# Performance work log

Hardware: AMD Instinct MI355X
Metric: run time of the kernel (lower is better)

## Reference

```python
import jax, jax.numpy as jnp
import numpy as np

B, N_O, N_Q = 2, 512, 512
POS_DIM, LATENT, HEADS, HEAD_DIM, OUT_DIM = 3, 256, 8, 32, 128
HD = HEADS * HEAD_DIM  # == LATENT here


def _lin(key, fan_in, fan_out):
    return jax.random.normal(key, (fan_in, fan_out), jnp.float32) / np.sqrt(fan_in)


def setup_inputs() -> dict:
    key = jax.random.key(0)
    ks = jax.random.split(key, 12)
    return {
        'h_obs': jax.random.normal(ks[0], (B, N_O, LATENT), jnp.float32),
        'pos_obs': jax.random.uniform(ks[1], (B, N_O, POS_DIM), jnp.float32),
        'pos_query': jax.random.uniform(ks[2], (B, N_Q, POS_DIM), jnp.float32),
        'fw1': _lin(ks[3], LATENT, LATENT), 'fb1': jnp.zeros((LATENT,), jnp.float32),
        'fw2': _lin(ks[4], LATENT, HD), 'fb2': jnp.zeros((HD,), jnp.float32),
        'log_sigma': jnp.zeros((HEADS,), jnp.float32),
        'kw1': _lin(ks[5], POS_DIM * 3, LATENT), 'kb1': jnp.zeros((LATENT,), jnp.float32),
        'kw2': _lin(ks[6], LATENT, HEADS), 'kb2': jnp.zeros((HEADS,), jnp.float32),
        'ow': _lin(ks[7], HD, OUT_DIM), 'ob': jnp.zeros((OUT_DIM,), jnp.float32),
        'vw': _lin(ks[8], HD, OUT_DIM), 'vb': jnp.zeros((OUT_DIM,), jnp.float32),
    }


def reference(h_obs, pos_obs, pos_query, fw1, fb1, fw2, fb2, log_sigma,
              kw1, kb1, kw2, kb2, ow, ob, vw, vb):
    Bv, No, _ = h_obs.shape
    Nq = pos_query.shape[1]
    # feature net -> values [B, H, N_o, D]
    v = jax.nn.relu(h_obs @ fw1 + fb1) @ fw2 + fb2
    v = v.reshape(Bv, No, HEADS, HEAD_DIM).transpose(0, 2, 1, 3)
    # pairwise relative positions [B, Nq, No, P]
    pos_q = pos_query[:, :, None, :]
    pos_o = pos_obs[:, None, :, :]
    rel = pos_q - pos_o
    dist2 = jnp.sum(rel ** 2, axis=-1)  # [B, Nq, No]
    sigma = jnp.exp(log_sigma)[None, :, None, None]
    rbf = jnp.exp(-dist2[:, None] / (sigma ** 2 + 1e-6))  # [B, H, Nq, No]
    # kernel MLP on concatenated pairwise positions [B, Nq, No, 3P] -> [B, H, Nq, No]
    ki = jnp.concatenate([
        jnp.broadcast_to(pos_q, (Bv, Nq, No, POS_DIM)),
        jnp.broadcast_to(pos_o, (Bv, Nq, No, POS_DIM)),
        rel], axis=-1)
    delta = (jax.nn.relu(ki @ kw1 + kb1) @ kw2 + kb2).transpose(0, 3, 1, 2)
    logits = jnp.log(rbf + 1e-8) + delta
    weights = jax.nn.softmax(logits, axis=-1)  # [B, H, Nq, No]
    # weighted mean over observations
    v_mean = jnp.einsum('bhqo,bhod->bhqd', weights, v)  # [B, H, Nq, D]
    h_query = v_mean.transpose(0, 2, 1, 3).reshape(Bv, Nq, HD)
    # weighted variance: sum_o w * (v_o - v_mean)^2
    residual = v[:, :, None, :, :] - v_mean[:, :, :, None, :]  # [B, H, Nq, No, D]
    var = jnp.sum(weights[..., None] * residual ** 2, axis=3)  # [B, H, Nq, D]
    var = var.transpose(0, 2, 1, 3).reshape(Bv, Nq, HD)
    mean = h_query @ ow + ob
    var_out = jax.nn.softplus(var @ vw + vb)
    return (mean, var_out)
```

## Files before the change

### kernel.cpp

```cpp
#include <hip/hip_runtime.h>
#include <math.h>

#define NB 2
#define NO 512
#define NQ 512
#define OUT_DIM 128
#define LPAD 516

typedef __attribute__((ext_vector_type(8))) _Float16 half8;
typedef __attribute__((ext_vector_type(4))) _Float16 half4;
typedef __attribute__((ext_vector_type(4))) float f32x4;

__device__ __forceinline__ float softplus_f(float x) {
  return x > 0.0f ? x + log1pf(expf(-x)) : log1pf(expf(x));
}
__device__ __forceinline__ int cvt2h(float x, float y) {
  return __builtin_bit_cast(int, __builtin_amdgcn_cvt_pkrtz(x, y));
}

__global__ __launch_bounds__(1024) void prep_kernel(
    const float* __restrict__ h_obs, const float* __restrict__ fw1,
    const float* __restrict__ fb1, const float* __restrict__ fw2,
    const float* __restrict__ fb2, const float* __restrict__ pos_obs,
    const float* __restrict__ kw1,
    _Float16* __restrict__ VT,
    _Float16* __restrict__ VT2,
    _Float16* __restrict__ AO_h)
{
  if (blockIdx.x < 256) {
    __shared__ float s_red[4][4][256];
    __shared__ float s_hid[4][256];
    const int n  = threadIdx.x & 255;
    const int ks = threadIdx.x >> 8;
    const int r0 = blockIdx.x * 4;
    const int k0 = ks * 64;
    float a0 = 0.f, a1 = 0.f, a2 = 0.f, a3 = 0.f;
    #pragma unroll 8
    for (int kk = 0; kk < 64; ++kk) {
      int k = k0 + kk;
      float w = fw1[k * 256 + n];
      a0 = fmaf(h_obs[(r0 + 0) * 256 + k], w, a0);
      a1 = fmaf(h_obs[(r0 + 1) * 256 + k], w, a1);
      a2 = fmaf(h_obs[(r0 + 2) * 256 + k], w, a2);
      a3 = fmaf(h_obs[(r0 + 3) * 256 + k], w, a3);
    }
    s_red[ks][0][n] = a0; s_red[ks][1][n] = a1;
    s_red[ks][2][n] = a2; s_red[ks][3][n] = a3;
    __syncthreads();
    if (ks == 0) {
      float bb = fb1[n];
      #pragma unroll
      for (int r = 0; r < 4; ++r) {
        float v = s_red[0][r][n] + s_red[1][r][n] + s_red[2][r][n] + s_red[3][r][n] + bb;
        s_hid[r][n] = fmaxf(v, 0.f);
      }
    }
    __syncthreads();
    float c0 = 0.f, c1 = 0.f, c2 = 0.f, c3 = 0.f;
    #pragma unroll 8
    for (int kk = 0; kk < 64; ++kk) {
      int k = k0 + kk;
      float w = fw2[k * 256 + n];
      c0 = fmaf(s_hid[0][k], w, c0);
      c1 = fmaf(s_hid[1][k], w, c1);
      c2 = fmaf(s_hid[2][k], w, c2);
      c3 = fmaf(s_hid[3][k], w, c3);
    }
    __syncthreads();
    s_red[ks][0][n] = c0; s_red[ks][1][n] = c1;
    s_red[ks][2][n] = c2; s_red[ks][3][n] = c3;
    __syncthreads();
    if (ks == 0) {
      float bb = fb2[n];
      float vr[4];
      #pragma unroll
      for (int r = 0; r < 4; ++r)
        vr[r] = s_red[0][r][n] + s_red[1][r][n] + s_red[2][r][n] + s_red[3][r][n] + bb;
      const int h  = n >> 5, d = n & 31;
      const int bb_ = r0 >> 9, o0 = r0 & 511;
      half4 pv, pv2;
      #pragma unroll
      for (int r = 0; r < 4; ++r) {
        pv[r]  = (_Float16)vr[r];
        pv2[r] = (_Float16)(vr[r] * vr[r]);
      }
      const size_t idx = ((size_t)((bb_ * 8 + h) * 32 + d)) * 512 + o0;
      *(half4*)(VT  + idx) = pv;
      *(half4*)(VT2 + idx) = pv2;
    }
  } else {
    const int i  = blockIdx.x - 256;
    const int b  = i >> 7;
    const int og = i & 127;
    const int ol = threadIdx.x >> 8;
    const int j  = threadIdx.x & 255;
    const int o  = og * 4 + ol;
    float c0 = kw1[3 * 256 + j] - kw1[6 * 256 + j];
    float c1 = kw1[4 * 256 + j] - kw1[7 * 256 + j];
    float c2 = kw1[5 * 256 + j] - kw1[8 * 256 + j];
    const float* p = pos_obs + ((size_t)(b * NO + o)) * 3;
    AO_h[(size_t)(b * NO + o) * 256 + j] =
        (_Float16)(fmaf(p[0], c0, fmaf(p[1], c1, p[2] * c2)));
  }
}

__global__ __launch_bounds__(512, 4) void attn_fused(
    const _Float16* __restrict__ VT,
    const _Float16* __restrict__ VT2,
    const _Float16* __restrict__ AO_h,
    const float* __restrict__ kw1,
    const float* __restrict__ kb1,
    const float* __restrict__ kw2,
    const float* __restrict__ kb2,
    const float* __restrict__ log_sigma,
    const float* __restrict__ pos_obs,
    const float* __restrict__ pos_query,
    const float* __restrict__ ow, const float* __restrict__ obias,
    const float* __restrict__ vw, const float* __restrict__ vbias,
    float* __restrict__ out)
{
  __shared__ __align__(16) float s_logits[2][8 * LPAD];
  __shared__ half8 s_Bh[512];
  __shared__ __align__(16) float s_pool[2048];

  _Float16* s_aq2 = (_Float16*)s_pool;
  float*    s_hv  = s_pool;
  float*    s_pred = s_pool + 1024;

  const int t   = threadIdx.x;
  const int bq0 = blockIdx.x * 2;
  const int b   = bq0 >> 9;

  float pqx[2], pqy[2], pqz[2];
  #pragma unroll
  for (int q = 0; q < 2; ++q) {
    pqx[q] = pos_query[(bq0 + q) * 3 + 0];
    pqy[q] = pos_query[(bq0 + q) * 3 + 1];
    pqz[q] = pos_query[(bq0 + q) * 3 + 2];
  }
  {
    const int q = t >> 8, j = t & 255;
    float c0 = kw1[0 * 256 + j] + kw1[6 * 256 + j];
    float c1 = kw1[1 * 256 + j] + kw1[7 * 256 + j];
    float c2 = kw1[2 * 256 + j] + kw1[8 * 256 + j];
    s_aq2[q * 256 + j] = (_Float16)
        fmaf(pqx[q], c0, fmaf(pqy[q], c1, fmaf(pqz[q], c2, kb1[j])));
  }
  {
    const int o = t;
    const float* p = pos_obs + (size_t)(b * NO + o) * 3;
    float px = p[0], py = p[1], pz = p[2];
    float d2q[2];
    #pragma unroll
    for (int q = 0; q < 2; ++q) {
      float r0 = pqx[q] - px, r1 = pqy[q] - py, r2 = pqz[q] - pz;
      d2q[q] = r0 * r0 + r1 * r1 + r2 * r2;
    }
    #pragma unroll
    for (int h = 0; h < 8; ++h) {
      float sg  = __expf(log_sigma[h]);
      float inv = 1.0f / (sg * sg + 1e-6f);
      float kbv = kb2[h];
      s_logits[0][h * LPAD + o] = __logf(__expf(-d2q[0] * inv) + 1e-8f) + kbv;
      s_logits[1][h * LPAD + o] = __logf(__expf(-d2q[1] * inv) + 1e-8f) + kbv;
    }
  }
  {
    const int kstep = t >> 6, lane = t & 63;
    const int nh = lane & 15;
    const int kb_ = kstep * 32 + ((lane >> 4) & 3) * 8;
    half8 b8;
    #pragma unroll
    for (int i = 0; i < 8; ++i) {
      float v = (nh < 8) ? kw2[(kb_ + i) * 8 + nh] : 0.f;
      b8[i] = (_Float16)v;
    }
    s_Bh[kstep * 64 + lane] = b8;
  }
  __syncthreads();

  {
    const int wave = t >> 6, lane = t & 63;
    const int quad = lane >> 4, mrow = lane & 15;
    const int tb   = wave * 4;
    f32x4 C[2][4];
    #pragma unroll
    for (int q = 0; q < 2; ++q)
      #pragma unroll
      for (int jt = 0; jt < 4; ++jt) C[q][jt] = (f32x4){0.f, 0.f, 0.f, 0.f};

    const half8 z8 = {0, 0, 0, 0, 0, 0, 0, 0};
    for (int kstep = 0; kstep < 8; ++kstep) {
      const int koff = kstep * 32 + quad * 8;
      half8 aq0 = *(const half8*)(s_aq2 + koff);
      half8 aq1 = *(const half8*)(s_aq2 + 256 + koff);
      half8 bh  = s_Bh[kstep * 64 + lane];
      #pragma unroll
      for (int jt = 0; jt < 4; ++jt) {
        const int o = (tb + jt) * 16 + mrow;
        half8 ao = *(const half8*)(AO_h + ((size_t)(b * NO + o) << 8) + koff);
        half8 a0 = __builtin_elementwise_max(aq0 + ao, z8);
        half8 a1 = __builtin_elementwise_max(aq1 + ao, z8);
        C[0][jt] = __builtin_amdgcn_mfma_f32_16x16x32_f16(a0, bh, C[0][jt], 0, 0, 0);
        C[1][jt] = __builtin_amdgcn_mfma_f32_16x16x32_f16(a1, bh, C[1][jt], 0, 0, 0);
      }
    }
    const int hh = lane & 15;
    if (hh < 8) {
      #pragma unroll
      for (int q = 0; q < 2; ++q)
        #pragma unroll
        for (int jt = 0; jt < 4; ++jt) {
          const int ob2 = (tb + jt) * 16 + quad * 4;
          #pragma unroll
          for (int r = 0; r < 4; ++r)
            s_logits[q][hh * LPAD + ob2 + r] += C[q][jt][r];
        }
    }
  }
  __syncthreads();

  {
    const int h = t >> 6, lane = t & 63;
    float invq[2];
    #pragma unroll
    for (int q = 0; q < 2; ++q) {
      float* pl = &s_logits[q][h * LPAD];
      float l8[8];
      float m = -1e30f;
      #pragma unroll
      for (int k = 0; k < 8; ++k) {
        l8[k] = pl[k * 64 + lane];
        m = fmaxf(m, l8[k]);
      }
      #pragma unroll
      for (int off = 32; off >= 1; off >>= 1) m = fmaxf(m, __shfl_xor(m, off, 64));
      float s = 0.f;
      #pragma unroll
      for (int k = 0; k < 8; ++k) {
        float p = __expf(l8[k] - m);
        pl[k * 64 + lane] = p;
        s += p;
      }
      #pragma unroll
      for (int off = 32; off >= 1; off >>= 1) s += __shfl_xor(s, off, 64);
      invq[q] = 1.0f / s;
    }
    const int nq = lane & 15, kg = lane >> 4, dl = lane & 15;
    const size_t vbase = ((size_t)(b * 8 + h) * 32 + dl) * 512;
    const _Float16* vt1 = VT  + vbase;
    const _Float16* vt2 = VT2 + vbase;
    const float* P = &s_logits[nq & 1][h * LPAD];
    f32x4 Cm0 = {0.f,0.f,0.f,0.f}, Cm1 = Cm0, Cv0 = Cm0, Cv1 = Cm0;
    #pragma unroll 4
    for (int ks = 0; ks < 16; ++ks) {
      const int ob = ks * 32 + kg * 8;
      float4 p0 = *(const float4*)(P + ob);
      float4 p1 = *(const float4*)(P + ob + 4);
      int4 bi;
      bi.x = cvt2h(p0.x, p0.y); bi.y = cvt2h(p0.z, p0.w);
      bi.z = cvt2h(p1.x, p1.y); bi.w = cvt2h(p1.z, p1.w);
      half8 bh = __builtin_bit_cast(half8, bi);
      half8 am0 = *(const half8*)(vt1 + ob);
      half8 am1 = *(const half8*)(vt1 + 8192 + ob);
      half8 av0 = *(const half8*)(vt2 + ob);
      half8 av1 = *(const half8*)(vt2 + 8192 + ob);
      Cm0 = __builtin_amdgcn_mfma_f32_16x16x32_f16(am0, bh, Cm0, 0, 0, 0);
      Cm1 = __builtin_amdgcn_mfma_f32_16x16x32_f16(am1, bh, Cm1, 0, 0, 0);
      Cv0 = __builtin_amdgcn_mfma_f32_16x16x32_f16(av0, bh, Cv0, 0, 0, 0);
      Cv1 = __builtin_amdgcn_mfma_f32_16x16x32_f16(av1, bh, Cv1, 0, 0, 0);
    }
    if (nq < 2) {
      const float iv = nq ? invq[1] : invq[0];
      const int dbase = h * 32 + kg * 4;
      f32x4 m0, v0, m1, v1;
      #pragma unroll
      for (int r = 0; r < 4; ++r) {
        float a = Cm0[r] * iv;
        m0[r] = a; v0[r] = fmaxf(Cv0[r] * iv - a * a, 0.f);
        float c = Cm1[r] * iv;
        m1[r] = c; v1[r] = fmaxf(Cv1[r] * iv - c * c, 0.f);
      }
      *(f32x4*)(s_hv + (nq * 2 + 0) * 256 + dbase)      = m0;
      *(f32x4*)(s_hv + (nq * 2 + 1) * 256 + dbase)      = v0;
      *(f32x4*)(s_hv + (nq * 2 + 0) * 256 + dbase + 16) = m1;
      *(f32x4*)(s_hv + (nq * 2 + 1) * 256 + dbase + 16) = v1;
    }
  }
  __syncthreads();

  {
    const int ks = t >> 8, mode = (t >> 7) & 1, n = t & 127;
    const float* W  = mode ? vw : ow;
    const float* X0 = s_hv + mode * 256;
    const float* X1 = s_hv + (2 + mode) * 256;
    float a0 = 0.f, a1 = 0.f;
    const int k0 = ks * 128;
    #pragma unroll 4
    for (int k = k0; k < k0 + 128; k += 4) {
      float4 x0 = *(const float4*)&X0[k];
      float4 x1 = *(const float4*)&X1[k];
      float w0 = W[(k + 0) * 128 + n];
      float w1 = W[(k + 1) * 128 + n];
      float w2 = W[(k + 2) * 128 + n];
      float w3 = W[(k + 3) * 128 + n];
      a0 = fmaf(x0.x, w0, a0); a1 = fmaf(x1.x, w0, a1);
      a0 = fmaf(x0.y, w1, a0); a1 = fmaf(x1.y, w1, a1);
      a0 = fmaf(x0.z, w2, a0); a1 = fmaf(x1.z, w2, a1);
      a0 = fmaf(x0.w, w3, a0); a1 = fmaf(x1.w, w3, a1);
    }
    s_pred[((ks * 2 + mode) * 2 + 0) * 128 + n] = a0;
    s_pred[((ks * 2 + mode) * 2 + 1) * 128 + n] = a1;
  }
  __syncthreads();
  {
    const int q = t >> 8, mode = (t >> 7) & 1, n = t & 127;
    float v = s_pred[((0 * 2 + mode) * 2 + q) * 128 + n]
            + s_pred[((1 * 2 + mode) * 2 + q) * 128 + n]
            + (mode ? vbias[n] : obias[n]);
    if (mode) v = softplus_f(v);
    out[(size_t)mode * (NB * NQ * OUT_DIM) + (size_t)(bq0 + q) * OUT_DIM + n] = v;
  }
}

extern "C" void kernel_launch(void* const* d_in, const int* in_sizes, int n_in,
                              void* d_out, int out_size, void* d_ws, size_t ws_size,
                              hipStream_t stream)
{
  const float* h_obs     = (const float*)d_in[0];
  const float* pos_obs   = (const float*)d_in[1];
  const float* pos_query = (const float*)d_in[2];
  const float* fw1       = (const float*)d_in[3];
  const float* fb1       = (const float*)d_in[4];
  const float* fw2       = (const float*)d_in[5];
  const float* fb2       = (const float*)d_in[6];
  const float* log_sigma = (const float*)d_in[7];
  const float* kw1       = (const float*)d_in[8];
  const float* kb1       = (const float*)d_in[9];
  const float* kw2       = (const float*)d_in[10];
  const float* kb2       = (const float*)d_in[11];
  const float* ow        = (const float*)d_in[12];
  const float* ob        = (const float*)d_in[13];
  const float* vw        = (const float*)d_in[14];
  const float* vb        = (const float*)d_in[15];

  float* out = (float*)d_out;
  _Float16* ws = (_Float16*)d_ws;

  _Float16* AO_h = ws;
  _Float16* VT   = ws + 262144;
  _Float16* VT2  = ws + 524288;

  prep_kernel<<<512, 1024, 0, stream>>>(h_obs, fw1, fb1, fw2, fb2,
                                        pos_obs, kw1, VT, VT2, AO_h);
  attn_fused<<<NB * NQ / 2, 512, 0, stream>>>(VT, VT2, AO_h, kw1, kb1, kw2, kb2,
                                              log_sigma, pos_obs, pos_query,
                                              ow, ob, vw, vb, out);
}
```

Measured before the change: 155.2 us.

## Recompute obs kernel features and V^2 on the fly, stage V via async LDS loads

Drops the precomputed AO_h and VT2 workspace buffers. The per-observation kernel-MLP term is now rebuilt in registers from pos_obs and coefficients held in shared memory, and V squared is computed in registers from V. Probabilities are stored once as fp16 in shared memory, and V tiles are streamed with global_load_lds into a ring of buffers paced by explicit vmcnt waits. This cuts global traffic and the prep kernel's work, but adds half-precision ALU work, an extra barrier, and fragile manual wait counts.

```diff
diff --git a/kernel.cpp b/kernel.cpp
--- a/kernel.cpp
+++ b/kernel.cpp
@@ -14,100 +14,85 @@
 __device__ __forceinline__ float softplus_f(float x) {
   return x > 0.0f ? x + log1pf(expf(-x)) : log1pf(expf(x));
 }
-__device__ __forceinline__ int cvt2h(float x, float y) {
-  return __builtin_bit_cast(int, __builtin_amdgcn_cvt_pkrtz(x, y));
+__device__ __forceinline__ half8 splat8(_Float16 v) {
+  return (half8){v, v, v, v, v, v, v, v};
+}
+__device__ __forceinline__ half8 fma8(half8 a, half8 b, half8 c) {
+  return __builtin_elementwise_fma(a, b, c);
+}
+__device__ __forceinline__ half8 max8(half8 a, half8 b) {
+  return __builtin_elementwise_max(a, b);
+}
+__device__ __forceinline__ void gll16(const void* g, void* l) {
+  __builtin_amdgcn_global_load_lds(
+      (const __attribute__((address_space(1))) unsigned int*)g,
+      (__attribute__((address_space(3))) unsigned int*)l, 16, 0, 0);
 }
 
 __global__ __launch_bounds__(1024) void prep_kernel(
     const float* __restrict__ h_obs, const float* __restrict__ fw1,
     const float* __restrict__ fb1, const float* __restrict__ fw2,
-    const float* __restrict__ fb2, const float* __restrict__ pos_obs,
-    const float* __restrict__ kw1,
-    _Float16* __restrict__ VT,
-    _Float16* __restrict__ VT2,
-    _Float16* __restrict__ AO_h)
+    const float* __restrict__ fb2, _Float16* __restrict__ VT)
 {
-  if (blockIdx.x < 256) {
-    __shared__ float s_red[4][4][256];
-    __shared__ float s_hid[4][256];
-    const int n  = threadIdx.x & 255;
-    const int ks = threadIdx.x >> 8;
-    const int r0 = blockIdx.x * 4;
-    const int k0 = ks * 64;
-    float a0 = 0.f, a1 = 0.f, a2 = 0.f, a3 = 0.f;
-    #pragma unroll 8
-    for (int kk = 0; kk < 64; ++kk) {
-      int k = k0 + kk;
-      float w = fw1[k * 256 + n];
-      a0 = fmaf(h_obs[(r0 + 0) * 256 + k], w, a0);
-      a1 = fmaf(h_obs[(r0 + 1) * 256 + k], w, a1);
-      a2 = fmaf(h_obs[(r0 + 2) * 256 + k], w, a2);
-      a3 = fmaf(h_obs[(r0 + 3) * 256 + k], w, a3);
-    }
-    s_red[ks][0][n] = a0; s_red[ks][1][n] = a1;
-    s_red[ks][2][n] = a2; s_red[ks][3][n] = a3;
-    __syncthreads();
-    if (ks == 0) {
-      float bb = fb1[n];
-      #pragma unroll
-      for (int r = 0; r < 4; ++r) {
-        float v = s_red[0][r][n] + s_red[1][r][n] + s_red[2][r][n] + s_red[3][r][n] + bb;
-        s_hid[r][n] = fmaxf(v, 0.f);
-      }
-    }
-    __syncthreads();
-    float c0 = 0.f, c1 = 0.f, c2 = 0.f, c3 = 0.f;
-    #pragma unroll 8
-    for (int kk = 0; kk < 64; ++kk) {
-      int k = k0 + kk;
-      float w = fw2[k * 256 + n];
-      c0 = fmaf(s_hid[0][k], w, c0);
-      c1 = fmaf(s_hid[1][k], w, c1);
-      c2 = fmaf(s_hid[2][k], w, c2);
-      c3 = fmaf(s_hid[3][k], w, c3);
-    }
-    __syncthreads();
-    s_red[ks][0][n] = c0; s_red[ks][1][n] = c1;
-    s_red[ks][2][n] = c2; s_red[ks][3][n] = c3;
-    __syncthreads();
-    if (ks == 0) {
-      float bb = fb2[n];
-      float vr[4];
-      #pragma unroll
-      for (int r = 0; r < 4; ++r)
-        vr[r] = s_red[0][r][n] + s_red[1][r][n] + s_red[2][r][n] + s_red[3][r][n] + bb;
-      const int h  = n >> 5, d = n & 31;
-      const int bb_ = r0 >> 9, o0 = r0 & 511;
-      half4 pv, pv2;
-      #pragma unroll
-      for (int r = 0; r < 4; ++r) {
-        pv[r]  = (_Float16)vr[r];
-        pv2[r] = (_Float16)(vr[r] * vr[r]);
-      }
-      const size_t idx = ((size_t)((bb_ * 8 + h) * 32 + d)) * 512 + o0;
-      *(half4*)(VT  + idx) = pv;
-      *(half4*)(VT2 + idx) = pv2;
-    }
-  } else {
-    const int i  = blockIdx.x - 256;
-    const int b  = i >> 7;
-    const int og = i & 127;
-    const int ol = threadIdx.x >> 8;
-    const int j  = threadIdx.x & 255;
-    const int o  = og * 4 + ol;
-    float c0 = kw1[3 * 256 + j] - kw1[6 * 256 + j];
-    float c1 = kw1[4 * 256 + j] - kw1[7 * 256 + j];
-    float c2 = kw1[5 * 256 + j] - kw1[8 * 256 + j];
-    const float* p = pos_obs + ((size_t)(b * NO + o)) * 3;
-    AO_h[(size_t)(b * NO + o) * 256 + j] =
-        (_Float16)(fmaf(p[0], c0, fmaf(p[1], c1, p[2] * c2)));
+  __shared__ float s_red[4][4][256];
+  __shared__ float s_hid[4][256];
+  const int n  = threadIdx.x & 255;
+  const int ks = threadIdx.x >> 8;
+  const int r0 = blockIdx.x * 4;
+  const int k0 = ks * 64;
+  float a0 = 0.f, a1 = 0.f, a2 = 0.f, a3 = 0.f;
+  #pragma unroll 8
+  for (int kk = 0; kk < 64; ++kk) {
+    int k = k0 + kk;
+    float w = fw1[k * 256 + n];
+    a0 = fmaf(h_obs[(r0 + 0) * 256 + k], w, a0);
+    a1 = fmaf(h_obs[(r0 + 1) * 256 + k], w, a1);
+    a2 = fmaf(h_obs[(r0 + 2) * 256 + k], w, a2);
+    a3 = fmaf(h_obs[(r0 + 3) * 256 + k], w, a3);
+  }
+  s_red[ks][0][n] = a0; s_red[ks][1][n] = a1;
+  s_red[ks][2][n] = a2; s_red[ks][3][n] = a3;
+  __syncthreads();
+  if (ks == 0) {
+    float bb = fb1[n];
+    #pragma unroll
+    for (int r = 0; r < 4; ++r) {
+      float v = s_red[0][r][n] + s_red[1][r][n] + s_red[2][r][n] + s_red[3][r][n] + bb;
+      s_hid[r][n] = fmaxf(v, 0.f);
+    }
+  }
+  __syncthreads();
+  float c0 = 0.f, c1 = 0.f, c2 = 0.f, c3 = 0.f;
+  #pragma unroll 8
+  for (int kk = 0; kk < 64; ++kk) {
+    int k = k0 + kk;
+    float w = fw2[k * 256 + n];
+    c0 = fmaf(s_hid[0][k], w, c0);
+    c1 = fmaf(s_hid[1][k], w, c1);
+    c2 = fmaf(s_hid[2][k], w, c2);
+    c3 = fmaf(s_hid[3][k], w, c3);
+  }
+  __syncthreads();
+  s_red[ks][0][n] = c0; s_red[ks][1][n] = c1;
+  s_red[ks][2][n] = c2; s_red[ks][3][n] = c3;
+  __syncthreads();
+  if (ks == 0) {
+    float bb = fb2[n];
+    float vr[4];
+    #pragma unroll
+    for (int r = 0; r < 4; ++r)
+      vr[r] = s_red[0][r][n] + s_red[1][r][n] + s_red[2][r][n] + s_red[3][r][n] + bb;
+    const int h  = n >> 5, d = n & 31;
+    const int bb_ = r0 >> 9, o0 = r0 & 511;
+    half4 pv;
+    #pragma unroll
+    for (int r = 0; r < 4; ++r) pv[r] = (_Float16)vr[r];
+    *(half4*)(VT + ((size_t)((bb_ * 8 + h) * 32 + d)) * 512 + o0) = pv;
   }
 }
 
 __global__ __launch_bounds__(512, 4) void attn_fused(
     const _Float16* __restrict__ VT,
-    const _Float16* __restrict__ VT2,
-    const _Float16* __restrict__ AO_h,
     const float* __restrict__ kw1,
     const float* __restrict__ kb1,
     const float* __restrict__ kw2,
@@ -120,11 +105,14 @@
     float* __restrict__ out)
 {
   __shared__ __align__(16) float s_logits[2][8 * LPAD];
+  __shared__ __align__(16) _Float16 s_P16[2][8][520];
   __shared__ half8 s_Bh[512];
   __shared__ __align__(16) float s_pool[2048];
+  __shared__ __align__(16) float s_po[3][516];
+  __shared__ __align__(16) _Float16 s_co[3][264];
 
   _Float16* s_aq2 = (_Float16*)s_pool;
-  float*    s_hv  = s_pool;
+  float*    s_hv   = s_pool;
   float*    s_pred = s_pool + 1024;
 
   const int t   = threadIdx.x;
@@ -146,10 +134,17 @@
     s_aq2[q * 256 + j] = (_Float16)
         fmaf(pqx[q], c0, fmaf(pqy[q], c1, fmaf(pqz[q], c2, kb1[j])));
   }
+  if (t < 256) {
+    const int j = t;
+    s_co[0][j] = (_Float16)(kw1[3 * 256 + j] - kw1[6 * 256 + j]);
+    s_co[1][j] = (_Float16)(kw1[4 * 256 + j] - kw1[7 * 256 + j]);
+    s_co[2][j] = (_Float16)(kw1[5 * 256 + j] - kw1[8 * 256 + j]);
+  }
   {
     const int o = t;
     const float* p = pos_obs + (size_t)(b * NO + o) * 3;
     float px = p[0], py = p[1], pz = p[2];
+    s_po[0][o] = px; s_po[1][o] = py; s_po[2][o] = pz;
     float d2q[2];
     #pragma unroll
     for (int q = 0; q < 2; ++q) {
@@ -183,6 +178,14 @@
     const int wave = t >> 6, lane = t & 63;
     const int quad = lane >> 4, mrow = lane & 15;
     const int tb   = wave * 4;
+    _Float16 pxh[4], pyh[4], pzh[4];
+    #pragma unroll
+    for (int jt = 0; jt < 4; ++jt) {
+      const int o = (tb + jt) * 16 + mrow;
+      pxh[jt] = (_Float16)s_po[0][o];
+      pyh[jt] = (_Float16)s_po[1][o];
+      pzh[jt] = (_Float16)s_po[2][o];
+    }
     f32x4 C[2][4];
     #pragma unroll
     for (int q = 0; q < 2; ++q)
@@ -190,17 +193,21 @@
       for (int jt = 0; jt < 4; ++jt) C[q][jt] = (f32x4){0.f, 0.f, 0.f, 0.f};
 
     const half8 z8 = {0, 0, 0, 0, 0, 0, 0, 0};
+    #pragma unroll
     for (int kstep = 0; kstep < 8; ++kstep) {
       const int koff = kstep * 32 + quad * 8;
+      half8 c0 = *(const half8*)&s_co[0][koff];
+      half8 c1 = *(const half8*)&s_co[1][koff];
+      half8 c2 = *(const half8*)&s_co[2][koff];
       half8 aq0 = *(const half8*)(s_aq2 + koff);
       half8 aq1 = *(const half8*)(s_aq2 + 256 + koff);
       half8 bh  = s_Bh[kstep * 64 + lane];
       #pragma unroll
       for (int jt = 0; jt < 4; ++jt) {
-        const int o = (tb + jt) * 16 + mrow;
-        half8 ao = *(const half8*)(AO_h + ((size_t)(b * NO + o) << 8) + koff);
-        half8 a0 = __builtin_elementwise_max(aq0 + ao, z8);
-        half8 a1 = __builtin_elementwise_max(aq1 + ao, z8);
+        half8 ao = fma8(splat8(pxh[jt]), c0,
+                   fma8(splat8(pyh[jt]), c1, splat8(pzh[jt]) * c2));
+        half8 a0 = max8(aq0 + ao, z8);
+        half8 a1 = max8(aq1 + ao, z8);
         C[0][jt] = __builtin_amdgcn_mfma_f32_16x16x32_f16(a0, bh, C[0][jt], 0, 0, 0);
         C[1][jt] = __builtin_amdgcn_mfma_f32_16x16x32_f16(a1, bh, C[1][jt], 0, 0, 0);
       }
@@ -239,39 +246,48 @@
       #pragma unroll
       for (int k = 0; k < 8; ++k) {
         float p = __expf(l8[k] - m);
-        pl[k * 64 + lane] = p;
         s += p;
+        s_P16[q][h][k * 64 + lane] = (_Float16)p;
       }
       #pragma unroll
       for (int off = 32; off >= 1; off >>= 1) s += __shfl_xor(s, off, 64);
       invq[q] = 1.0f / s;
     }
-    const int nq = lane & 15, kg = lane >> 4, dl = lane & 15;
-    const size_t vbase = ((size_t)(b * 8 + h) * 32 + dl) * 512;
-    const _Float16* vt1 = VT  + vbase;
-    const _Float16* vt2 = VT2 + vbase;
-    const float* P = &s_logits[nq & 1][h * LPAD];
-    f32x4 Cm0 = {0.f,0.f,0.f,0.f}, Cm1 = Cm0, Cv0 = Cm0, Cv1 = Cm0;
-    #pragma unroll 4
+    __syncthreads();
+
+    const int kg = lane >> 4, dl = lane & 15;
+    char* stg = (char*)s_logits + h * 4096;
+    const _Float16* vt = VT + ((size_t)(b * 8 + h) << 14);
+    const _Float16* vsrc = vt + (lane >> 1) * 512 + (lane & 1) * 8;
+    #define STAGE(j) gll16(vsrc + (j) * 16, stg + ((j) & 3) * 1024)
+    STAGE(0); STAGE(1); STAGE(2); STAGE(3);
+
+    const _Float16* pB = &s_P16[lane & 1][h][0];
+    f32x4 Cm0 = {0.f, 0.f, 0.f, 0.f}, Cm1 = Cm0, Cv0 = Cm0, Cv1 = Cm0;
+    #pragma unroll
     for (int ks = 0; ks < 16; ++ks) {
-      const int ob = ks * 32 + kg * 8;
-      float4 p0 = *(const float4*)(P + ob);
-      float4 p1 = *(const float4*)(P + ob + 4);
-      int4 bi;
-      bi.x = cvt2h(p0.x, p0.y); bi.y = cvt2h(p0.z, p0.w);
-      bi.z = cvt2h(p1.x, p1.y); bi.w = cvt2h(p1.z, p1.w);
-      half8 bh = __builtin_bit_cast(half8, bi);
-      half8 am0 = *(const half8*)(vt1 + ob);
-      half8 am1 = *(const half8*)(vt1 + 8192 + ob);
-      half8 av0 = *(const half8*)(vt2 + ob);
-      half8 av1 = *(const half8*)(vt2 + 8192 + ob);
-      Cm0 = __builtin_amdgcn_mfma_f32_16x16x32_f16(am0, bh, Cm0, 0, 0, 0);
-      Cm1 = __builtin_amdgcn_mfma_f32_16x16x32_f16(am1, bh, Cm1, 0, 0, 0);
-      Cv0 = __builtin_amdgcn_mfma_f32_16x16x32_f16(av0, bh, Cv0, 0, 0, 0);
-      Cv1 = __builtin_amdgcn_mfma_f32_16x16x32_f16(av1, bh, Cv1, 0, 0, 0);
-    }
+      if (ks < 15) asm volatile("s_waitcnt vmcnt(2)" ::: "memory");
+      else         asm volatile("s_waitcnt vmcnt(0)" ::: "memory");
+      const char* bufc = stg + ((2 * ks + (kg >> 1)) & 3) * 1024
+                       + dl * 32 + (kg & 1) * 16;
+      half8 am0 = *(const half8*)(bufc);
+      half8 am1 = *(const half8*)(bufc + 512);
+      half8 pb  = *(const half8*)(pB + ks * 32 + kg * 8);
+      half8 av0 = am0 * am0;
+      half8 av1 = am1 * am1;
+      Cm0 = __builtin_amdgcn_mfma_f32_16x16x32_f16(am0, pb, Cm0, 0, 0, 0);
+      Cm1 = __builtin_amdgcn_mfma_f32_16x16x32_f16(am1, pb, Cm1, 0, 0, 0);
+      Cv0 = __builtin_amdgcn_mfma_f32_16x16x32_f16(av0, pb, Cv0, 0, 0, 0);
+      Cv1 = __builtin_amdgcn_mfma_f32_16x16x32_f16(av1, pb, Cv1, 0, 0, 0);
+      if (ks < 14) {
+        asm volatile("s_waitcnt lgkmcnt(0)" ::: "memory");
+        STAGE(2 * ks + 4); STAGE(2 * ks + 5);
+      }
+    }
+    #undef STAGE
+    const int nq = lane & 15;
     if (nq < 2) {
-      const float iv = nq ? invq[1] : invq[0];
+      const float iv = invq[nq];
       const int dbase = h * 32 + kg * 4;
       f32x4 m0, v0, m1, v1;
       #pragma unroll
@@ -345,15 +361,10 @@
   const float* vb        = (const float*)d_in[15];
 
   float* out = (float*)d_out;
-  _Float16* ws = (_Float16*)d_ws;
-
-  _Float16* AO_h = ws;
-  _Float16* VT   = ws + 262144;
-  _Float16* VT2  = ws + 524288;
-
-  prep_kernel<<<512, 1024, 0, stream>>>(h_obs, fw1, fb1, fw2, fb2,
-                                        pos_obs, kw1, VT, VT2, AO_h);
-  attn_fused<<<NB * NQ / 2, 512, 0, stream>>>(VT, VT2, AO_h, kw1, kb1, kw2, kb2,
+  _Float16* VT = (_Float16*)d_ws;
+
+  prep_kernel<<<256, 1024, 0, stream>>>(h_obs, fw1, fb1, fw2, fb2, VT);
+  attn_fused<<<NB * NQ / 2, 512, 0, stream>>>(VT, kw1, kb1, kw2, kb2,
                                               log_sigma, pos_obs, pos_query,
                                               ow, ob, vw, vb, out);
 }
```

New measurement: 127.7 us. -17.8%, faster.
